# Kernel tuning notes

Hardware: AMD Instinct MI355X
Metric: run time of the kernel (lower is better)

## Reference

```python
import jax, jax.numpy as jnp
import numpy as np

C = 256
CQK = max(C // 8, 1)  # 32
B, H, W = 4, 64, 64


def setup_inputs() -> dict:
    key = jax.random.key(0)
    ks = jax.random.split(key, 8)
    s = 0.02
    return {
        "x": jax.random.normal(ks[0], (B, C, H, W), dtype=jnp.float32),
        "Wq": jax.random.normal(ks[1], (CQK, C), dtype=jnp.float32) * s,
        "bq": jax.random.normal(ks[2], (CQK,), dtype=jnp.float32) * s,
        "Wk": jax.random.normal(ks[3], (CQK, C), dtype=jnp.float32) * s,
        "bk": jax.random.normal(ks[4], (CQK,), dtype=jnp.float32) * s,
        "Wv": jax.random.normal(ks[5], (C, C), dtype=jnp.float32) * s,
        "bv": jax.random.normal(ks[6], (C,), dtype=jnp.float32) * s,
        "gamma": jax.random.normal(ks[7], (1,), dtype=jnp.float32) * 0.1,
    }


def reference(x, Wq, bq, Wk, bk, Wv, bv, gamma):
    b, c, h, w = x.shape
    n = h * w
    xf = x.reshape(b, c, n)  # [B,C,N]
    # 1x1 convs == per-pixel linear projections
    q = jnp.einsum("qc,bcn->bqn", Wq, xf) + bq[None, :, None]  # [B,Cqk,N]
    k = jnp.einsum("qc,bcn->bqn", Wk, xf) + bk[None, :, None]  # [B,Cqk,N]
    v = jnp.einsum("vc,bcn->bvn", Wv, xf) + bv[None, :, None]  # [B,C,N]
    # attention[b,i,j] = sum_q K[b,q,i] * Q[b,q,j], softmax over j
    attn = jax.nn.softmax(jnp.einsum("bqi,bqj->bij", k, q), axis=-1)  # [B,N,N]
    # out[b,c,m] = sum_n V[b,c,n] * attn[b,m,n]
    out = jnp.einsum("bcn,bmn->bcm", v, attn).reshape(b, c, h, w)
    return gamma[0] * out + x
```

## Files before the change

kernel.cpp:

```cpp
#include <hip/hip_runtime.h>
#include <hip/hip_bf16.h>


#define BB 4
#define CC 256
#define NN 4096
#define CQ 32

typedef __hip_bfloat16 bf16;
typedef __attribute__((ext_vector_type(8))) short short8;
typedef __attribute__((ext_vector_type(4))) short short4v;
typedef __attribute__((ext_vector_type(4))) float f32x4;

__device__ __forceinline__ unsigned short f2b(float f) {
  unsigned u = __builtin_bit_cast(unsigned, f);
  return (unsigned short)((u + 0x7FFFu + ((u >> 16) & 1u)) >> 16);
}
__device__ __forceinline__ float b2f(unsigned short s) {
  return __builtin_bit_cast(float, (unsigned)s << 16);
}

__global__ __launch_bounds__(512)
void wcast_kernel(const float* __restrict__ Wq, const float* __restrict__ Wk,
                  const float* __restrict__ Wv,
                  bf16* __restrict__ Wqk, bf16* __restrict__ Wvb)
{
  const int base = blockIdx.x * 5120 + threadIdx.x;
#pragma unroll
  for (int j = 0; j < 10; ++j) {
    const int i = base + j * 512;
    if (i < 8192)        ((short*)Wqk)[i]         = (short)f2b(Wq[i]);
    else if (i < 16384)  ((short*)Wqk)[i]         = (short)f2b(Wk[i - 8192]);
    else                 ((short*)Wvb)[i - 16384] = (short)f2b(Wv[i - 16384]);
  }
}

__global__ __launch_bounds__(512)
void proj_fused(const float* __restrict__ x,
                const bf16* __restrict__ Wqk, const bf16* __restrict__ Wvb,
                const float* __restrict__ bq, const float* __restrict__ bk,
                const float* __restrict__ bv,
                bf16* __restrict__ Qt, bf16* __restrict__ Kt,
                bf16* __restrict__ Vn)
{
  __shared__ short xts[32 * 264];
  const int tid  = threadIdx.x;
  const int b    = blockIdx.x >> 7;
  const int n0   = (blockIdx.x & 127) * 32;
  const int w    = tid >> 6;
  const int lane = tid & 63;
  const int l15  = lane & 15;
  const int hi   = lane >> 4;

  {
    const int n  = tid & 31;
    const int cp = tid >> 5;
    const float* xb = x + (size_t)b * CC * NN + n0 + n;
#pragma unroll
    for (int j = 0; j < 8; ++j) {
      const int c0 = j * 32 + cp * 2;
      const float v0 = xb[(size_t)c0 * NN];
      const float v1 = xb[(size_t)(c0 + 1) * NN];
      const unsigned pk = (unsigned)f2b(v0) | ((unsigned)f2b(v1) << 16);
      *(unsigned*)&xts[n * 264 + c0] = pk;
    }
  }
  __syncthreads();

  {
    const int ccol = w & 3;
    const int nrow = w >> 2;
    const short* wrow = (const short*)Wqk + (size_t)(ccol * 16 + l15) * CC + hi * 8;
    const short* arow = &xts[(nrow * 16 + l15) * 264 + hi * 8];
    f32x4 acc = {0.f, 0.f, 0.f, 0.f};
#pragma unroll
    for (int k = 0; k < 8; ++k) {
      short8 a  = *(const short8*)(arow + k * 32);
      short8 bb = *(const short8*)(wrow + k * 32);
      acc = __builtin_amdgcn_mfma_f32_16x16x32_bf16(a, bb, acc, 0, 0, 0);
    }
    const int cq = (ccol & 1) * 16 + l15;
    const float bias = (ccol < 2) ? bq[cq] : bk[cq];
    short* dst = (short*)((ccol < 2) ? Qt : Kt);
#pragma unroll
    for (int rg = 0; rg < 4; ++rg) {
      const int n = n0 + nrow * 16 + hi * 4 + rg;
      dst[((size_t)b * NN + n) * CQ + cq] = (short)f2b(acc[rg] + bias);
    }
  }

#pragma unroll
  for (int cc = 0; cc < 2; ++cc) {
    const int ct = w * 2 + cc;
    const short* wrow = (const short*)Wvb + (size_t)(ct * 16 + l15) * CC + hi * 8;
    short8 af[8];
#pragma unroll
    for (int k = 0; k < 8; ++k) af[k] = *(const short8*)(wrow + k * 32);
    const f32x4 bvv = *(const f32x4*)(bv + ct * 16 + hi * 4);
#pragma unroll
    for (int nt2 = 0; nt2 < 2; ++nt2) {
      const short* brow = &xts[(nt2 * 16 + l15) * 264 + hi * 8];
      f32x4 acc = {0.f, 0.f, 0.f, 0.f};
#pragma unroll
      for (int k = 0; k < 8; ++k) {
        short8 bb = *(const short8*)(brow + k * 32);
        acc = __builtin_amdgcn_mfma_f32_16x16x32_bf16(af[k], bb, acc, 0, 0, 0);
      }
#pragma unroll
      for (int rg = 0; rg < 4; ++rg) {
        const int c = ct * 16 + hi * 4 + rg;
        ((short*)Vn)[((size_t)b * CC + c) * NN + n0 + nt2 * 16 + l15] =
            (short)f2b(acc[rg] + bvv[rg]);
      }
    }
  }
}

template <int SPLIT>
__global__ __launch_bounds__(256)
void flash_kernel(const bf16* __restrict__ Qt, const bf16* __restrict__ Kt,
                  const bf16* __restrict__ Vn, const float* __restrict__ x,
                  const float* __restrict__ gamma, float* __restrict__ outp,
                  bf16* __restrict__ o1, float* __restrict__ lp, int ntl)
{
  __shared__ short vlds[CC * 64];
  __shared__ short plds[4 * 16 * 72];
  __shared__ float llds[64];

  const int tid  = threadIdx.x;
  const int w    = tid >> 6;
  const int lane = tid & 63;
  const int l15  = lane & 15;
  const int hi   = lane >> 4;
  const int b    = blockIdx.x >> 6;
  const int mt   = blockIdx.x & 63;
  const int m0   = mt * 64 + w * 16;
  const int h    = SPLIT ? (int)blockIdx.y : 0;
  const int t0   = h * ntl;

  const short8 a_k =
      *(const short8*)((const short*)Kt + ((size_t)b * NN + m0 + l15) * CQ + hi * 8);

  f32x4 acc[4][4];
#pragma unroll
  for (int i = 0; i < 4; ++i)
#pragma unroll
    for (int j = 0; j < 4; ++j) acc[i][j] = f32x4{0.f, 0.f, 0.f, 0.f};

  float l_run[4] = {0.f, 0.f, 0.f, 0.f};

  const int r8  = lane >> 3, c8 = lane & 7;
  const int swz = 8 * (c8 ^ r8);

  auto stage = [&](int t) {
    const short* vb = (const short*)Vn + (size_t)b * CC * NN + t * 64;
#pragma unroll
    for (int i = 0; i < 8; ++i) {
      const int rowb = i * 32 + w * 8;
      const short* src = vb + (size_t)(rowb + r8) * NN + swz;
      short* dst = &vlds[rowb * 64];
      __builtin_amdgcn_global_load_lds(
          (const __attribute__((address_space(1))) unsigned int*)src,
          (__attribute__((address_space(3))) unsigned int*)dst, 16, 0, 0);
    }
  };

  auto loadQ = [&](int t, short8* q) {
    const short* qb = (const short*)Qt + ((size_t)b * NN + t * 64) * CQ;
#pragma unroll
    for (int tt = 0; tt < 4; ++tt)
      q[tt] = *(const short8*)(qb + (tt * 16 + l15) * CQ + hi * 8);
  };

  short8 qf[4];
  loadQ(t0, qf);
  stage(t0);

  for (int ti = 0; ti < ntl; ++ti) {
    f32x4 s[4];
#pragma unroll
    for (int tt = 0; tt < 4; ++tt) {
      f32x4 z = {0.f, 0.f, 0.f, 0.f};
      s[tt] = __builtin_amdgcn_mfma_f32_16x16x32_bf16(a_k, qf[tt], z, 0, 0, 0);
    }
    short8 qn[4];
    if (ti + 1 < ntl) loadQ(t0 + ti + 1, qn);

    float p[4][4];
#pragma unroll
    for (int r = 0; r < 4; ++r) {
      float rs = 0.f;
#pragma unroll
      for (int tt = 0; tt < 4; ++tt) { p[tt][r] = __expf(s[tt][r]); rs += p[tt][r]; }
      rs += __shfl_xor(rs, 1, 64);
      rs += __shfl_xor(rs, 2, 64);
      rs += __shfl_xor(rs, 4, 64);
      rs += __shfl_xor(rs, 8, 64);
      l_run[r] += rs;
    }
#pragma unroll
    for (int tt = 0; tt < 4; ++tt)
#pragma unroll
      for (int r = 0; r < 4; ++r)
        plds[(w * 16 + hi * 4 + r) * 72 + tt * 16 + l15] = (short)f2b(p[tt][r]);
    __syncthreads();

    short8 af[4][2];
#pragma unroll
    for (int mq = 0; mq < 4; ++mq)
#pragma unroll
      for (int kk = 0; kk < 2; ++kk)
        af[mq][kk] = *(const short8*)&plds[(mq * 16 + l15) * 72 + kk * 32 + hi * 8];
    __builtin_amdgcn_s_setprio(1);
#pragma unroll
    for (int ci = 0; ci < 4; ++ci) {
      const int c16 = (w * 4 + ci) * 16;
#pragma unroll
      for (int kk = 0; kk < 2; ++kk) {
        short8 bv = *(const short8*)
            &vlds[(c16 + l15) * 64 + ((kk * 32 + hi * 8) ^ (8 * (l15 & 7)))];
#pragma unroll
        for (int mq = 0; mq < 4; ++mq)
          acc[ci][mq] = __builtin_amdgcn_mfma_f32_16x16x32_bf16(af[mq][kk], bv,
                                                               acc[ci][mq], 0, 0, 0);
      }
    }
    __builtin_amdgcn_s_setprio(0);
    __syncthreads();
    if (ti + 1 < ntl) stage(t0 + ti + 1);
#pragma unroll
    for (int tt = 0; tt < 4; ++tt) qf[tt] = qn[tt];
  }

  if (SPLIT == 0) {
    if (l15 == 0) {
      f32x4 lv = {l_run[0], l_run[1], l_run[2], l_run[3]};
      *(f32x4*)&llds[w * 16 + hi * 4] = lv;
    }
    __syncthreads();
    const float g0 = gamma[0];
#pragma unroll
    for (int mq = 0; mq < 4; ++mq) {
      f32x4 lv = *(const f32x4*)&llds[mq * 16 + hi * 4];
      f32x4 inv;
#pragma unroll
      for (int r = 0; r < 4; ++r) inv[r] = 1.f / lv[r];
#pragma unroll
      for (int ci = 0; ci < 4; ++ci) {
        const int c = (w * 4 + ci) * 16 + l15;
        const size_t base = ((size_t)(b * CC + c)) * NN + (size_t)mt * 64 + mq * 16 + hi * 4;
        f32x4 xv = *(const f32x4*)(x + base);
        f32x4 o;
#pragma unroll
        for (int r = 0; r < 4; ++r) o[r] = g0 * (acc[ci][mq][r] * inv[r]) + xv[r];
        *(f32x4*)(outp + base) = o;
      }
    }
  } else {
    if (l15 == 0) {
      f32x4 lv = {l_run[0], l_run[1], l_run[2], l_run[3]};
      *(f32x4*)&lp[(size_t)(h * BB + b) * NN + m0 + hi * 4] = lv;
    }
    const size_t slot = (size_t)(h - 1) * BB * CC * NN;
#pragma unroll
    for (int mq = 0; mq < 4; ++mq) {
#pragma unroll
      for (int ci = 0; ci < 4; ++ci) {
        const int c = (w * 4 + ci) * 16 + l15;
        const size_t base = ((size_t)(b * CC + c)) * NN + (size_t)mt * 64 + mq * 16 + hi * 4;
        if (h == 0) {
          *(f32x4*)(outp + base) = acc[ci][mq];
        } else {
          short4v o;
#pragma unroll
          for (int r = 0; r < 4; ++r) o[r] = (short)f2b(acc[ci][mq][r]);
          *(short4v*)((short*)o1 + slot + base) = o;
        }
      }
    }
  }
}

template <int NH>
__global__ __launch_bounds__(256)
void merge_kernel(float* __restrict__ out, const bf16* __restrict__ o1,
                  const float* __restrict__ lp, const float* __restrict__ x,
                  const float* __restrict__ gamma)
{
  const size_t base = ((size_t)blockIdx.x * 256 + threadIdx.x) * 4;
  const int b = (int)(base / ((size_t)CC * NN));
  const int m = (int)(base % NN);

  f32x4 o = *(const f32x4*)(out + base);
  f32x4 l = *(const f32x4*)&lp[(size_t)b * NN + m];
#pragma unroll
  for (int hh = 1; hh < NH; ++hh) {
    short4v s = *(const short4v*)((const short*)o1 + (size_t)(hh - 1) * BB * CC * NN + base);
#pragma unroll
    for (int j = 0; j < 4; ++j) o[j] += b2f((unsigned short)s[j]);
    f32x4 lh = *(const f32x4*)&lp[(size_t)(hh * BB + b) * NN + m];
#pragma unroll
    for (int j = 0; j < 4; ++j) l[j] += lh[j];
  }
  const f32x4 xv = *(const f32x4*)(x + base);
  const float g = gamma[0];
  f32x4 r;
#pragma unroll
  for (int j = 0; j < 4; ++j) r[j] = g * (o[j] / l[j]) + xv[j];
  *(f32x4*)(out + base) = r;
}

extern "C" void kernel_launch(void* const* d_in, const int* in_sizes, int n_in,
                              void* d_out, int out_size, void* d_ws, size_t ws_size,
                              hipStream_t stream) {
  (void)in_sizes; (void)n_in; (void)out_size;
  const float* x     = (const float*)d_in[0];
  const float* Wq    = (const float*)d_in[1];
  const float* bq    = (const float*)d_in[2];
  const float* Wk    = (const float*)d_in[3];
  const float* bk    = (const float*)d_in[4];
  const float* Wv    = (const float*)d_in[5];
  const float* bv    = (const float*)d_in[6];
  const float* gamma = (const float*)d_in[7];
  float* out = (float*)d_out;

  char* ws = (char*)d_ws;
  const size_t SZ_Q   = (size_t)BB * NN * CQ * 2;
  const size_t SZ_V   = (size_t)BB * CC * NN * 2;
  const size_t SZ_WQK = 64 * 256 * 2;
  const size_t SZ_WVB = 256 * 256 * 2;
  const size_t SZ_LP  = (size_t)4 * BB * NN * 4;
  const size_t SZ_O1  = (size_t)BB * CC * NN * 2;

  bf16*  Qt  = (bf16*)ws;   ws += SZ_Q;
  bf16*  Kt  = (bf16*)ws;   ws += SZ_Q;
  bf16*  Vn  = (bf16*)ws;   ws += SZ_V;
  bf16*  Wqk = (bf16*)ws;   ws += SZ_WQK;
  bf16*  Wvb = (bf16*)ws;   ws += SZ_WVB;
  float* lp  = (float*)ws;  ws += SZ_LP;
  const size_t need_small = (size_t)(ws - (char*)d_ws);
  bf16*  O1  = (bf16*)ws;
  const size_t need_mid  = need_small + SZ_O1;
  const size_t need_full = need_small + 3 * SZ_O1;

  wcast_kernel<<<dim3(16), dim3(512), 0, stream>>>(Wq, Wk, Wv, Wqk, Wvb);
  proj_fused<<<dim3(512), dim3(512), 0, stream>>>(x, Wqk, Wvb, bq, bk, bv, Qt, Kt, Vn);

  if (ws_size >= need_full) {
    flash_kernel<1><<<dim3(256, 4), dim3(256), 0, stream>>>(Qt, Kt, Vn, x, gamma,
                                                            out, O1, lp, 16);
    merge_kernel<4><<<dim3(4096), dim3(256), 0, stream>>>(out, O1, lp, x, gamma);
  } else if (ws_size >= need_mid) {
    flash_kernel<1><<<dim3(256, 2), dim3(256), 0, stream>>>(Qt, Kt, Vn, x, gamma,
                                                            out, O1, lp, 32);
    merge_kernel<2><<<dim3(4096), dim3(256), 0, stream>>>(out, O1, lp, x, gamma);
  } else {
    flash_kernel<0><<<dim3(256, 1), dim3(256), 0, stream>>>(Qt, Kt, Vn, x, gamma,
                                                            out, O1, lp, 64);
  }
}
```

Before: 183.3 us.

## Coalesce V stores via LDS, swizzle P tile, defer row-sum reduction

The projection kernel now stages the V tile in shared memory, reusing the x buffer, and writes it to global memory as 16-byte vector rows instead of scattered 2-byte stores. The flash kernel drops the padded P buffer in favour of an XOR-swizzled 64-wide layout, which saves LDS while still avoiding bank conflicts. The per-tile cross-lane shuffle reduction of the softmax row sum is moved to a single reduction after the loop. A min-blocks-per-CU hint of 4 is added to launch_bounds, which may limit registers and cause spills.

Result: slower. 375.4 us (+104.8%).

```diff
diff --git a/kernel.cpp b/kernel.cpp
--- a/kernel.cpp
+++ b/kernel.cpp
@@ -43,7 +43,10 @@
                 bf16* __restrict__ Qt, bf16* __restrict__ Kt,
                 bf16* __restrict__ Vn)
 {
-  __shared__ short xts[32 * 264];
+  __shared__ __align__(16) short sbuf[256 * 40];
+  short* xts = sbuf;
+  short* vls = sbuf;
+
   const int tid  = threadIdx.x;
   const int b    = blockIdx.x >> 7;
   const int n0   = (blockIdx.x & 127) * 32;
@@ -89,6 +92,7 @@
     }
   }
 
+  f32x4 vacc[2][2];
 #pragma unroll
   for (int cc = 0; cc < 2; ++cc) {
     const int ct = w * 2 + cc;
@@ -107,25 +111,42 @@
         acc = __builtin_amdgcn_mfma_f32_16x16x32_bf16(af[k], bb, acc, 0, 0, 0);
       }
 #pragma unroll
-      for (int rg = 0; rg < 4; ++rg) {
-        const int c = ct * 16 + hi * 4 + rg;
-        ((short*)Vn)[((size_t)b * CC + c) * NN + n0 + nt2 * 16 + l15] =
-            (short)f2b(acc[rg] + bvv[rg]);
-      }
-    }
+      for (int rg = 0; rg < 4; ++rg) acc[rg] += bvv[rg];
+      vacc[cc][nt2] = acc;
+    }
+  }
+  __syncthreads();
+
+#pragma unroll
+  for (int cc = 0; cc < 2; ++cc) {
+    const int ct = w * 2 + cc;
+#pragma unroll
+    for (int nt2 = 0; nt2 < 2; ++nt2)
+#pragma unroll
+      for (int rg = 0; rg < 4; ++rg)
+        vls[(ct * 16 + hi * 4 + rg) * 40 + nt2 * 16 + l15] =
+            (short)f2b(vacc[cc][nt2][rg]);
+  }
+  __syncthreads();
+
+  {
+    const int c = tid >> 1, seg = tid & 1;
+    short* dst = (short*)Vn + ((size_t)(b * CC + c)) * NN + n0 + seg * 16;
+    const short* src = &vls[c * 40 + seg * 16];
+    *(short8*)(dst)     = *(const short8*)(src);
+    *(short8*)(dst + 8) = *(const short8*)(src + 8);
   }
 }
 
 template <int SPLIT>
-__global__ __launch_bounds__(256)
+__global__ __launch_bounds__(256, 4)
 void flash_kernel(const bf16* __restrict__ Qt, const bf16* __restrict__ Kt,
                   const bf16* __restrict__ Vn, const float* __restrict__ x,
                   const float* __restrict__ gamma, float* __restrict__ outp,
                   bf16* __restrict__ o1, float* __restrict__ lp, int ntl)
 {
-  __shared__ short vlds[CC * 64];
-  __shared__ short plds[4 * 16 * 72];
-  __shared__ float llds[64];
+  __shared__ __align__(16) short vlds[CC * 64];
+  __shared__ __align__(16) short plds[64 * 64];
 
   const int tid  = threadIdx.x;
   const int w    = tid >> 6;
@@ -186,31 +207,27 @@
     short8 qn[4];
     if (ti + 1 < ntl) loadQ(t0 + ti + 1, qn);
 
-    float p[4][4];
-#pragma unroll
-    for (int r = 0; r < 4; ++r) {
-      float rs = 0.f;
-#pragma unroll
-      for (int tt = 0; tt < 4; ++tt) { p[tt][r] = __expf(s[tt][r]); rs += p[tt][r]; }
-      rs += __shfl_xor(rs, 1, 64);
-      rs += __shfl_xor(rs, 2, 64);
-      rs += __shfl_xor(rs, 4, 64);
-      rs += __shfl_xor(rs, 8, 64);
-      l_run[r] += rs;
-    }
-#pragma unroll
-    for (int tt = 0; tt < 4; ++tt)
-#pragma unroll
-      for (int r = 0; r < 4; ++r)
-        plds[(w * 16 + hi * 4 + r) * 72 + tt * 16 + l15] = (short)f2b(p[tt][r]);
+#pragma unroll
+    for (int tt = 0; tt < 4; ++tt) {
+#pragma unroll
+      for (int r = 0; r < 4; ++r) {
+        const float pv = __expf(s[tt][r]);
+        l_run[r] += pv;
+        const int row = w * 16 + hi * 4 + r;
+        plds[row * 64 + ((tt * 16 + l15) ^ ((row & 7) * 8))] = (short)f2b(pv);
+      }
+    }
     __syncthreads();
 
     short8 af[4][2];
 #pragma unroll
     for (int mq = 0; mq < 4; ++mq)
 #pragma unroll
-      for (int kk = 0; kk < 2; ++kk)
-        af[mq][kk] = *(const short8*)&plds[(mq * 16 + l15) * 72 + kk * 32 + hi * 8];
+      for (int kk = 0; kk < 2; ++kk) {
+        const int row = mq * 16 + l15;
+        af[mq][kk] = *(const short8*)
+            &plds[row * 64 + ((kk * 32 + hi * 8) ^ ((row & 7) * 8))];
+      }
     __builtin_amdgcn_s_setprio(1);
 #pragma unroll
     for (int ci = 0; ci < 4; ++ci) {
@@ -232,7 +249,16 @@
     for (int tt = 0; tt < 4; ++tt) qf[tt] = qn[tt];
   }
 
+#pragma unroll
+  for (int r = 0; r < 4; ++r) {
+    l_run[r] += __shfl_xor(l_run[r], 1, 64);
+    l_run[r] += __shfl_xor(l_run[r], 2, 64);
+    l_run[r] += __shfl_xor(l_run[r], 4, 64);
+    l_run[r] += __shfl_xor(l_run[r], 8, 64);
+  }
+
   if (SPLIT == 0) {
+    float* llds = (float*)vlds;
     if (l15 == 0) {
       f32x4 lv = {l_run[0], l_run[1], l_run[2], l_run[3]};
       *(f32x4*)&llds[w * 16 + hi * 4] = lv;
```
